# Performance work log

Hardware: AMD Instinct MI355X
Metric: run time of the kernel (lower is better)

## Reference

```python
import jax, jax.numpy as jnp
import numpy as np

EMBED = 1024
FF = 4096
HEADS = 16
HEAD_SIZE = EMBED // HEADS


def setup_inputs() -> dict:
    key = jax.random.key(0)
    ks = jax.random.split(key, 12)
    s = 0.02
    inp = {
        "x": jax.random.normal(ks[0], (2, 2048, EMBED), dtype=jnp.float32),
        "Wq": jax.random.normal(ks[1], (EMBED, EMBED), dtype=jnp.float32) * s,
        "bq": jnp.zeros((EMBED,), jnp.float32),
        "Wk": jax.random.normal(ks[2], (EMBED, EMBED), dtype=jnp.float32) * s,
        "bk": jnp.zeros((EMBED,), jnp.float32),
        "Wv": jax.random.normal(ks[3], (EMBED, EMBED), dtype=jnp.float32) * s,
        "bv": jnp.zeros((EMBED,), jnp.float32),
        "Wo": jax.random.normal(ks[4], (EMBED, EMBED), dtype=jnp.float32) * s,
        "bo": jnp.zeros((EMBED,), jnp.float32),
        "W1": jax.random.normal(ks[5], (EMBED, FF), dtype=jnp.float32) * s,
        "b1": jnp.zeros((FF,), jnp.float32),
        "W2": jax.random.normal(ks[6], (FF, EMBED), dtype=jnp.float32) * s,
        "b2": jnp.zeros((EMBED,), jnp.float32),
        "ln1_g": jnp.ones((EMBED,), jnp.float32),
        "ln1_b": jnp.zeros((EMBED,), jnp.float32),
        "ln2_g": jnp.ones((EMBED,), jnp.float32),
        "ln2_b": jnp.zeros((EMBED,), jnp.float32),
    }
    return inp


def _layernorm(x, g, b, eps=1e-5):
    mu = jnp.mean(x, axis=-1, keepdims=True)
    var = jnp.var(x, axis=-1, keepdims=True)
    return (x - mu) * jax.lax.rsqrt(var + eps) * g + b


def _attn(x, Wq, bq, Wk, bk, Wv, bv, Wo, bo):
    B, S, E = x.shape
    q = (x @ Wq + bq).reshape(B, S, HEADS, HEAD_SIZE)
    k = (x @ Wk + bk).reshape(B, S, HEADS, HEAD_SIZE)
    v = (x @ Wv + bv).reshape(B, S, HEADS, HEAD_SIZE)
    # full (non-causal) attention, scores materialized as in the original
    att = jnp.einsum('bqhd,bkhd->bhqk', q, k) / jnp.sqrt(jnp.float32(HEAD_SIZE))
    att = jax.nn.softmax(att, axis=-1)
    out = jnp.einsum('bhqk,bkhd->bqhd', att, v).reshape(B, S, E)
    return out @ Wo + bo


def reference(x, Wq, bq, Wk, bk, Wv, bv, Wo, bo, W1, b1, W2, b2,
              ln1_g, ln1_b, ln2_g, ln2_b):
    x = x + _attn(_layernorm(x, ln1_g, ln1_b), Wq, bq, Wk, bk, Wv, bv, Wo, bo)
    h = _layernorm(x, ln2_g, ln2_b)
    x = x + (jax.nn.gelu(h @ W1 + b1) @ W2 + b2)
    return x
```

## Files before the change

### kernel.cpp

```cpp
#include <hip/hip_runtime.h>

typedef __bf16 bf16;
typedef __bf16 bf16x8 __attribute__((ext_vector_type(8)));
typedef __bf16 bf16x4 __attribute__((ext_vector_type(4)));
typedef float f32x4 __attribute__((ext_vector_type(4)));

#define EMBED 1024
#define FFDIM 4096
#define HEADS 16
#define HD 64
#define SEQ 2048
#define BATCH 2
#define TOKENS (BATCH * SEQ)
#define MB (1u << 20)


__device__ __forceinline__ void gld16(const void* g, void* l) {
  __builtin_amdgcn_global_load_lds(
      (const __attribute__((address_space(1))) void*)g,
      (__attribute__((address_space(3))) void*)l, 16, 0, 0);
}

__device__ __forceinline__ float gelu_f(float x) {
  float u = 0.7978845608028654f * (x + 0.044715f * x * x * x);
  float t = tanhf(u);
  return 0.5f * x * (1.0f + t);
}

__device__ __forceinline__ void xcd_tiles(int nx, int& tx, int& ty) {
  int lid = blockIdx.x + nx * blockIdx.y;
  tx = (lid >> 3) % nx;
  ty = ((lid / (8 * nx)) << 3) | (lid & 7);
}

__global__ __launch_bounds__(256) void transpose_cast(const float* __restrict__ in,
                                                      bf16* __restrict__ out,
                                                      int R, int C) {
  __shared__ float t[32][33];
  int bx = blockIdx.x * 32;
  int by = blockIdx.y * 32;
  int tx = threadIdx.x & 31;
  int ty = threadIdx.x >> 5;
#pragma unroll
  for (int i = 0; i < 32; i += 8)
    t[ty + i][tx] = in[(size_t)(by + ty + i) * C + bx + tx];
  __syncthreads();
#pragma unroll
  for (int i = 0; i < 32; i += 8)
    out[(size_t)(bx + ty + i) * R + by + tx] = (bf16)t[tx][ty + i];
}

__global__ __launch_bounds__(256) void transpose_cast4(
    const float* __restrict__ W0, const float* __restrict__ W1,
    const float* __restrict__ W2, const float* __restrict__ W3,
    bf16* __restrict__ O0, bf16* __restrict__ O1,
    bf16* __restrict__ O2, bf16* __restrict__ O3) {
  const float* in;
  bf16* out;
  int z = blockIdx.z;
  if (z == 0) { in = W0; out = O0; }
  else if (z == 1) { in = W1; out = O1; }
  else if (z == 2) { in = W2; out = O2; }
  else { in = W3; out = O3; }
  __shared__ float t[32][33];
  int bx = blockIdx.x * 32;
  int by = blockIdx.y * 32;
  int tx = threadIdx.x & 31;
  int ty = threadIdx.x >> 5;
#pragma unroll
  for (int i = 0; i < 32; i += 8)
    t[ty + i][tx] = in[(size_t)(by + ty + i) * EMBED + bx + tx];
  __syncthreads();
#pragma unroll
  for (int i = 0; i < 32; i += 8)
    out[(size_t)(bx + ty + i) * EMBED + by + tx] = (bf16)t[tx][ty + i];
}

__global__ __launch_bounds__(256) void ln_kernel(const float* __restrict__ x,
                                                 const float* __restrict__ g,
                                                 const float* __restrict__ b,
                                                 bf16* __restrict__ out) {
  int tok = blockIdx.x;
  int tid = threadIdx.x;
  const float4* xv = (const float4*)(x + (size_t)tok * EMBED);
  float4 v = xv[tid];
  float s = v.x + v.y + v.z + v.w;
  float s2 = v.x * v.x + v.y * v.y + v.z * v.z + v.w * v.w;
#pragma unroll
  for (int off = 32; off >= 1; off >>= 1) {
    s += __shfl_xor(s, off, 64);
    s2 += __shfl_xor(s2, off, 64);
  }
  __shared__ float ps[4], ps2[4];
  int w = tid >> 6;
  if ((tid & 63) == 0) { ps[w] = s; ps2[w] = s2; }
  __syncthreads();
  s = ps[0] + ps[1] + ps[2] + ps[3];
  s2 = ps2[0] + ps2[1] + ps2[2] + ps2[3];
  float mu = s * (1.0f / EMBED);
  float var = s2 * (1.0f / EMBED) - mu * mu;
  float r = rsqrtf(var + 1e-5f);
  float4 gg = ((const float4*)g)[tid];
  float4 bb = ((const float4*)b)[tid];
  bf16x4 o;
  o[0] = (bf16)((v.x - mu) * r * gg.x + bb.x);
  o[1] = (bf16)((v.y - mu) * r * gg.y + bb.y);
  o[2] = (bf16)((v.z - mu) * r * gg.z + bb.z);
  o[3] = (bf16)((v.w - mu) * r * gg.w + bb.w);
  ((bf16x4*)(out + (size_t)tok * EMBED))[tid] = o;
}

template <int MODE>
__global__ __launch_bounds__(256) void gemm_bt(const bf16* __restrict__ A,
                                               const bf16* __restrict__ BT,
                                               const float* __restrict__ bias,
                                               void* __restrict__ out,
                                               int M, int N, int K,
                                               const float* __restrict__ bias2,
                                               const float* __restrict__ bias3,
                                               void* __restrict__ out2,
                                               void* __restrict__ out3) {
  __shared__ bf16 ldsA[128 * 64];
  __shared__ bf16 ldsB[128 * 64];
  int tid = threadIdx.x;
  int wave = tid >> 6, lane = tid & 63;
  int lquad = lane >> 4, l15 = lane & 15;
  int wm = wave >> 1, wn = wave & 1;
  int tileM = blockIdx.y * 128, tileN = blockIdx.x * 128;

  f32x4 acc[4][4];
#pragma unroll
  for (int i = 0; i < 4; i++)
#pragma unroll
    for (int j = 0; j < 4; j++) acc[i][j] = (f32x4){0.f, 0.f, 0.f, 0.f};

  int srow = lane >> 3;
  int sch = lane & 7;

  for (int k0 = 0; k0 < K; k0 += 64) {
    __syncthreads();
#pragma unroll
    for (int c = 0; c < 4; c++) {
      int base = wave * 32 + c * 8;
      int row = base + srow;
      int ch = sch ^ (row & 7);
      gld16(&A[(size_t)(tileM + row) * K + k0 + ch * 8], &ldsA[base * 64]);
      gld16(&BT[(size_t)(tileN + row) * K + k0 + ch * 8], &ldsB[base * 64]);
    }
    __syncthreads();

    bf16x8 aF[2][4], bF[2][4];
#pragma unroll
    for (int ks = 0; ks < 2; ks++) {
#pragma unroll
      for (int i = 0; i < 4; i++) {
        int R = wm * 64 + i * 16 + l15;
        int ch = (ks * 4 + lquad) ^ (R & 7);
        aF[ks][i] = *(const bf16x8*)&ldsA[R * 64 + ch * 8];
      }
#pragma unroll
      for (int j = 0; j < 4; j++) {
        int R = wn * 64 + j * 16 + l15;
        int ch = (ks * 4 + lquad) ^ (R & 7);
        bF[ks][j] = *(const bf16x8*)&ldsB[R * 64 + ch * 8];
      }
    }
#pragma unroll
    for (int i = 0; i < 4; i++)
#pragma unroll
      for (int j = 0; j < 4; j++)
#pragma unroll
        for (int ks = 0; ks < 2; ks++)
          acc[i][j] = __builtin_amdgcn_mfma_f32_16x16x32_bf16(aF[ks][i], bF[ks][j], acc[i][j], 0, 0, 0);
  }

  int r0 = tileM + wm * 64;
  int c0 = tileN + wn * 64;
#pragma unroll
  for (int i = 0; i < 4; i++) {
#pragma unroll
    for (int j = 0; j < 4; j++) {
      int col = c0 + j * 16 + l15;
      float bv;
      if (MODE == 4) {
        int sel = col >> 10, cc = col & 1023;
        bv = (sel == 0 ? bias : sel == 1 ? bias2 : bias3)[cc];
      } else {
        bv = bias[col];
      }
#pragma unroll
      for (int r = 0; r < 4; r++) {
        int row = r0 + i * 16 + lquad * 4 + r;
        float v = acc[i][j][r] + bv;
        if (MODE == 0) {
          ((bf16*)out)[(size_t)row * N + col] = (bf16)v;
        } else if (MODE == 3) {
          ((bf16*)out)[(size_t)row * N + col] = (bf16)gelu_f(v);
        } else {
          int sel = col >> 10, cc = col & 1023;
          if (sel == 0) {
            ((bf16*)out)[(size_t)row * EMBED + cc] = (bf16)v;
          } else if (sel == 1) {
            ((bf16*)out2)[(size_t)row * EMBED + cc] = (bf16)v;
          } else {
            int bb = row >> 11, s = row & (SEQ - 1);
            ((bf16*)out3)[((size_t)(bb * EMBED + cc)) * SEQ + s] = (bf16)v;
          }
        }
      }
    }
  }
}

__global__ __launch_bounds__(256) void gemm_bt64(const bf16* __restrict__ A,
                                                 const bf16* __restrict__ BT,
                                                 const float* __restrict__ bias,
                                                 const float* __restrict__ res,
                                                 float* __restrict__ out,
                                                 int M, int N, int K) {
  __shared__ bf16 ldsA[128 * 64];
  __shared__ bf16 ldsB[64 * 64];
  int tid = threadIdx.x;
  int wave = tid >> 6, lane = tid & 63;
  int lquad = lane >> 4, l15 = lane & 15;
  int wm = wave >> 1, wn = wave & 1;
  int txs, tys;
  xcd_tiles(N >> 6, txs, tys);
  int tileM = tys * 128, tileN = txs * 64;

  f32x4 acc[4][2];
#pragma unroll
  for (int i = 0; i < 4; i++)
#pragma unroll
    for (int j = 0; j < 2; j++) acc[i][j] = (f32x4){0.f, 0.f, 0.f, 0.f};

  int srow = lane >> 3;
  int sch = lane & 7;

  for (int k0 = 0; k0 < K; k0 += 64) {
    __syncthreads();
#pragma unroll
    for (int c = 0; c < 4; c++) {
      int base = wave * 32 + c * 8;
      int row = base + srow;
      int ch = sch ^ (row & 7);
      gld16(&A[(size_t)(tileM + row) * K + k0 + ch * 8], &ldsA[base * 64]);
    }
#pragma unroll
    for (int c = 0; c < 2; c++) {
      int base = wave * 16 + c * 8;
      int row = base + srow;
      int ch = sch ^ (row & 7);
      gld16(&BT[(size_t)(tileN + row) * K + k0 + ch * 8], &ldsB[base * 64]);
    }
    __syncthreads();

    bf16x8 aF[2][4], bF[2][2];
#pragma unroll
    for (int ks = 0; ks < 2; ks++) {
#pragma unroll
      for (int i = 0; i < 4; i++) {
        int R = wm * 64 + i * 16 + l15;
        int ch = (ks * 4 + lquad) ^ (R & 7);
        aF[ks][i] = *(const bf16x8*)&ldsA[R * 64 + ch * 8];
      }
#pragma unroll
      for (int j = 0; j < 2; j++) {
        int R = wn * 32 + j * 16 + l15;
        int ch = (ks * 4 + lquad) ^ (R & 7);
        bF[ks][j] = *(const bf16x8*)&ldsB[R * 64 + ch * 8];
      }
    }
#pragma unroll
    for (int i = 0; i < 4; i++)
#pragma unroll
      for (int j = 0; j < 2; j++)
#pragma unroll
        for (int ks = 0; ks < 2; ks++)
          acc[i][j] = __builtin_amdgcn_mfma_f32_16x16x32_bf16(aF[ks][i], bF[ks][j], acc[i][j], 0, 0, 0);
  }

  int r0 = tileM + wm * 64;
  int c0 = tileN + wn * 32;
#pragma unroll
  for (int i = 0; i < 4; i++) {
#pragma unroll
    for (int j = 0; j < 2; j++) {
      int col = c0 + j * 16 + l15;
      float bv = bias[col];
#pragma unroll
      for (int r = 0; r < 4; r++) {
        int row = r0 + i * 16 + lquad * 4 + r;
        out[(size_t)row * N + col] = acc[i][j][r] + bv + res[(size_t)row * N + col];
      }
    }
  }
}

__global__ __launch_bounds__(256) void attn_kernel(const bf16* __restrict__ q,
                                                   const bf16* __restrict__ k,
                                                   const bf16* __restrict__ vT,
                                                   bf16* __restrict__ o) {
  int lid = blockIdx.x;
  int qb = (lid >> 3) & 15;
  int g = (lid & 7) | ((lid >> 7) << 3);
  int h = g & 15, b = g >> 4;
  int tid = threadIdx.x;
  int w = tid >> 6, lane = tid & 63;
  int lquad = lane >> 4, l15 = lane & 15;

  __shared__ bf16 ldsK[128 * 64];
  __shared__ bf16 ldsV[64 * 128];
  __shared__ bf16 ldsP[4][16 * 136];

  bf16x8 qB[2][2];
#pragma unroll
  for (int f = 0; f < 2; f++) {
    int qrow = b * SEQ + qb * 128 + w * 32 + f * 16 + l15;
    qB[f][0] = *(const bf16x8*)&q[(size_t)qrow * EMBED + h * HD + lquad * 8];
    qB[f][1] = *(const bf16x8*)&q[(size_t)qrow * EMBED + h * HD + 32 + lquad * 8];
  }

  f32x4 O[2][4];
#pragma unroll
  for (int f = 0; f < 2; f++)
#pragma unroll
    for (int j = 0; j < 4; j++) O[f][j] = (f32x4){0.f, 0.f, 0.f, 0.f};
  float lsum[2] = {0.f, 0.f};
  const float C2 = 0.18033688011112042f;

  for (int kb = 0; kb < SEQ; kb += 128) {
    __syncthreads();
#pragma unroll
    for (int c = 0; c < 4; c++) {
      int base = w * 32 + c * 8;
      int row = base + (lane >> 3);
      int ch = (lane & 7) ^ (row & 7);
      gld16(&k[(size_t)(b * SEQ + kb + row) * EMBED + h * HD + ch * 8],
            &ldsK[base * 64]);
    }
#pragma unroll
    for (int c = 0; c < 4; c++) {
      int base = w * 16 + c * 4;
      int row = base + (lane >> 4);
      int ch = (lane & 15) ^ (row & 7);
      gld16(&vT[(size_t)(b * EMBED + h * HD + row) * SEQ + kb + ch * 8],
            &ldsV[base * 128]);
    }
    __syncthreads();

    f32x4 st[2][8];
#pragma unroll
    for (int t = 0; t < 8; t++) {
      st[0][t] = (f32x4){0.f, 0.f, 0.f, 0.f};
      st[1][t] = (f32x4){0.f, 0.f, 0.f, 0.f};
#pragma unroll
      for (int ks = 0; ks < 2; ks++) {
        int R = t * 16 + l15;
        int ch = (ks * 4 + lquad) ^ (R & 7);
        bf16x8 kA = *(const bf16x8*)&ldsK[R * 64 + ch * 8];
        st[0][t] = __builtin_amdgcn_mfma_f32_16x16x32_bf16(kA, qB[0][ks], st[0][t], 0, 0, 0);
        st[1][t] = __builtin_amdgcn_mfma_f32_16x16x32_bf16(kA, qB[1][ks], st[1][t], 0, 0, 0);
      }
    }

    bf16x8 pB[2][4];
#pragma unroll
    for (int f = 0; f < 2; f++) {
      float rs = 0.f;
#pragma unroll
      for (int t = 0; t < 8; t++) {
        bf16x4 pk;
#pragma unroll
        for (int r = 0; r < 4; r++) {
          float e = __builtin_amdgcn_exp2f(st[f][t][r] * C2);
          rs += e;
          pk[r] = (bf16)e;
        }
        *(bf16x4*)&ldsP[w][l15 * 136 + t * 16 + lquad * 4] = pk;
      }
      lsum[f] += rs;
#pragma unroll
      for (int ks2 = 0; ks2 < 4; ks2++)
        pB[f][ks2] = *(const bf16x8*)&ldsP[w][l15 * 136 + ks2 * 32 + lquad * 8];
    }

#pragma unroll
    for (int j = 0; j < 4; j++) {
#pragma unroll
      for (int ks2 = 0; ks2 < 4; ks2++) {
        int R = j * 16 + l15;
        int ch = (ks2 * 4 + lquad) ^ (R & 7);
        bf16x8 vA = *(const bf16x8*)&ldsV[R * 128 + ch * 8];
        O[0][j] = __builtin_amdgcn_mfma_f32_16x16x32_bf16(vA, pB[0][ks2], O[0][j], 0, 0, 0);
        O[1][j] = __builtin_amdgcn_mfma_f32_16x16x32_bf16(vA, pB[1][ks2], O[1][j], 0, 0, 0);
      }
    }
  }

#pragma unroll
  for (int f = 0; f < 2; f++) {
    float ls = lsum[f];
    ls += __shfl_xor(ls, 16, 64);
    ls += __shfl_xor(ls, 32, 64);
    float inv = 1.0f / ls;
    int tok = b * SEQ + qb * 128 + w * 32 + f * 16 + l15;
#pragma unroll
    for (int j = 0; j < 4; j++) {
      bf16x4 ov;
#pragma unroll
      for (int r = 0; r < 4; r++) ov[r] = (bf16)(O[f][j][r] * inv);
      *(bf16x4*)&o[(size_t)tok * EMBED + h * HD + j * 16 + lquad * 4] = ov;
    }
  }
}


extern "C" void kernel_launch(void* const* d_in, const int* in_sizes, int n_in,
                              void* d_out, int out_size, void* d_ws, size_t ws_size,
                              hipStream_t stream) {
  const float* x = (const float*)d_in[0];
  const float* Wq = (const float*)d_in[1];
  const float* bq = (const float*)d_in[2];
  const float* Wk = (const float*)d_in[3];
  const float* bk = (const float*)d_in[4];
  const float* Wv = (const float*)d_in[5];
  const float* bv = (const float*)d_in[6];
  const float* Wo = (const float*)d_in[7];
  const float* bo = (const float*)d_in[8];
  const float* W1 = (const float*)d_in[9];
  const float* b1 = (const float*)d_in[10];
  const float* W2 = (const float*)d_in[11];
  const float* b2 = (const float*)d_in[12];
  const float* ln1_g = (const float*)d_in[13];
  const float* ln1_b = (const float*)d_in[14];
  const float* ln2_g = (const float*)d_in[15];
  const float* ln2_b = (const float*)d_in[16];

  char* ws = (char*)d_ws;
  bf16* WqT = (bf16*)(ws + 0 * MB);
  bf16* WkT = (bf16*)(ws + 2 * MB);
  bf16* WvT = (bf16*)(ws + 4 * MB);
  bf16* WoT = (bf16*)(ws + 6 * MB);
  bf16* W1T = (bf16*)(ws + 8 * MB);
  bf16* W2T = (bf16*)(ws + 16 * MB);
  bf16* xn1 = (bf16*)(ws + 24 * MB);
  bf16* qbuf = (bf16*)(ws + 32 * MB);
  bf16* kbuf = (bf16*)(ws + 40 * MB);
  bf16* vT = (bf16*)(ws + 48 * MB);
  bf16* attnb = (bf16*)(ws + 56 * MB);
  float* x2f = (float*)(ws + 64 * MB);
  bf16* xn2 = (bf16*)(ws + 80 * MB);
  bf16* hb = (bf16*)(ws + 88 * MB);
  float* outf = (float*)d_out;

  transpose_cast4<<<dim3(32, 32, 4), 256, 0, stream>>>(Wq, Wk, Wv, Wo,
                                                       WqT, WkT, WvT, WoT);
  transpose_cast<<<dim3(128, 32), 256, 0, stream>>>(W1, W1T, EMBED, FFDIM);
  transpose_cast<<<dim3(32, 128), 256, 0, stream>>>(W2, W2T, FFDIM, EMBED);

  ln_kernel<<<TOKENS, 256, 0, stream>>>(x, ln1_g, ln1_b, xn1);

  gemm_bt<4><<<dim3(3072 / 128, TOKENS / 128), 256, 0, stream>>>(
      xn1, WqT, bq, qbuf, TOKENS, 3072, EMBED, bk, bv, kbuf, vT);

  attn_kernel<<<dim3(SEQ / 128 * HEADS * BATCH), 256, 0, stream>>>(qbuf, kbuf, vT, attnb);

  gemm_bt64<<<dim3(EMBED / 64, TOKENS / 128), 256, 0, stream>>>(
      attnb, WoT, bo, x, x2f, TOKENS, EMBED, EMBED);

  ln_kernel<<<TOKENS, 256, 0, stream>>>(x2f, ln2_g, ln2_b, xn2);

  gemm_bt<3><<<dim3(FFDIM / 128, TOKENS / 128), 256, 0, stream>>>(
      xn2, W1T, b1, hb, TOKENS, FFDIM, EMBED,
      nullptr, nullptr, nullptr, nullptr);
  gemm_bt64<<<dim3(EMBED / 64, TOKENS / 128), 256, 0, stream>>>(
      hb, W2T, b2, x2f, outf, TOKENS, EMBED, FFDIM);
}
```

Baseline: 372.7 us.

## Split-K the output GEMMs with atomic accumulation into LN-preinitialized residual buffers

Replaces the 128x64-tile output projection and FFN-down GEMMs with a 128x128-tile split-K (two halves) kernel that atomically adds partial sums into fp32 output. The LayerNorm kernels now also write residual+bias into the destination buffer, so the GEMM epilogue no longer reads the residual or bias. The intent is to raise per-tile reuse while keeping the block count up and to drop the residual reads. In exchange it adds fp32 atomic traffic, makes results depend on summation order, and removes the XCD-aware tile mapping.

```diff
diff --git a/kernel.cpp b/kernel.cpp
--- a/kernel.cpp
+++ b/kernel.cpp
@@ -25,12 +25,6 @@
   float u = 0.7978845608028654f * (x + 0.044715f * x * x * x);
   float t = tanhf(u);
   return 0.5f * x * (1.0f + t);
-}
-
-__device__ __forceinline__ void xcd_tiles(int nx, int& tx, int& ty) {
-  int lid = blockIdx.x + nx * blockIdx.y;
-  tx = (lid >> 3) % nx;
-  ty = ((lid / (8 * nx)) << 3) | (lid & 7);
 }
 
 __global__ __launch_bounds__(256) void transpose_cast(const float* __restrict__ in,
@@ -76,10 +70,12 @@
     out[(size_t)(bx + ty + i) * EMBED + by + tx] = (bf16)t[tx][ty + i];
 }
 
-__global__ __launch_bounds__(256) void ln_kernel(const float* __restrict__ x,
-                                                 const float* __restrict__ g,
-                                                 const float* __restrict__ b,
-                                                 bf16* __restrict__ out) {
+__global__ __launch_bounds__(256) void ln_fused(const float* __restrict__ x,
+                                                const float* __restrict__ g,
+                                                const float* __restrict__ b,
+                                                const float* __restrict__ bias2,
+                                                bf16* __restrict__ out,
+                                                float* __restrict__ init_out) {
   int tok = blockIdx.x;
   int tid = threadIdx.x;
   const float4* xv = (const float4*)(x + (size_t)tok * EMBED);
@@ -108,6 +104,10 @@
   o[2] = (bf16)((v.z - mu) * r * gg.z + bb.z);
   o[3] = (bf16)((v.w - mu) * r * gg.w + bb.w);
   ((bf16x4*)(out + (size_t)tok * EMBED))[tid] = o;
+  float4 i2 = ((const float4*)bias2)[tid];
+  float4 iv;
+  iv.x = v.x + i2.x; iv.y = v.y + i2.y; iv.z = v.z + i2.z; iv.w = v.w + i2.w;
+  ((float4*)(init_out + (size_t)tok * EMBED))[tid] = iv;
 }
 
 template <int MODE>
@@ -192,11 +192,9 @@
       for (int r = 0; r < 4; r++) {
         int row = r0 + i * 16 + lquad * 4 + r;
         float v = acc[i][j][r] + bv;
-        if (MODE == 0) {
-          ((bf16*)out)[(size_t)row * N + col] = (bf16)v;
-        } else if (MODE == 3) {
+        if (MODE == 3) {
           ((bf16*)out)[(size_t)row * N + col] = (bf16)gelu_f(v);
-        } else {
+        } else if (MODE == 4) {
           int sel = col >> 10, cc = col & 1023;
           if (sel == 0) {
             ((bf16*)out)[(size_t)row * EMBED + cc] = (bf16)v;
@@ -206,38 +204,38 @@
             int bb = row >> 11, s = row & (SEQ - 1);
             ((bf16*)out3)[((size_t)(bb * EMBED + cc)) * SEQ + s] = (bf16)v;
           }
+        } else {
+          ((bf16*)out)[(size_t)row * N + col] = (bf16)v;
         }
       }
     }
   }
 }
 
-__global__ __launch_bounds__(256) void gemm_bt64(const bf16* __restrict__ A,
-                                                 const bf16* __restrict__ BT,
-                                                 const float* __restrict__ bias,
-                                                 const float* __restrict__ res,
-                                                 float* __restrict__ out,
-                                                 int M, int N, int K) {
+__global__ __launch_bounds__(256) void gemm_sk(const bf16* __restrict__ A,
+                                               const bf16* __restrict__ BT,
+                                               float* __restrict__ out,
+                                               int M, int N, int K) {
   __shared__ bf16 ldsA[128 * 64];
-  __shared__ bf16 ldsB[64 * 64];
+  __shared__ bf16 ldsB[128 * 64];
   int tid = threadIdx.x;
   int wave = tid >> 6, lane = tid & 63;
   int lquad = lane >> 4, l15 = lane & 15;
   int wm = wave >> 1, wn = wave & 1;
-  int txs, tys;
-  xcd_tiles(N >> 6, txs, tys);
-  int tileM = tys * 128, tileN = txs * 64;
-
-  f32x4 acc[4][2];
+  int tileM = blockIdx.y * 128, tileN = blockIdx.x * 128;
+  int Kh = K >> 1;
+  int kbeg = blockIdx.z * Kh;
+
+  f32x4 acc[4][4];
 #pragma unroll
   for (int i = 0; i < 4; i++)
 #pragma unroll
-    for (int j = 0; j < 2; j++) acc[i][j] = (f32x4){0.f, 0.f, 0.f, 0.f};
+    for (int j = 0; j < 4; j++) acc[i][j] = (f32x4){0.f, 0.f, 0.f, 0.f};
 
   int srow = lane >> 3;
   int sch = lane & 7;
 
-  for (int k0 = 0; k0 < K; k0 += 64) {
+  for (int k0 = kbeg; k0 < kbeg + Kh; k0 += 64) {
     __syncthreads();
 #pragma unroll
     for (int c = 0; c < 4; c++) {
@@ -245,17 +243,11 @@
       int row = base + srow;
       int ch = sch ^ (row & 7);
       gld16(&A[(size_t)(tileM + row) * K + k0 + ch * 8], &ldsA[base * 64]);
-    }
-#pragma unroll
-    for (int c = 0; c < 2; c++) {
-      int base = wave * 16 + c * 8;
-      int row = base + srow;
-      int ch = sch ^ (row & 7);
       gld16(&BT[(size_t)(tileN + row) * K + k0 + ch * 8], &ldsB[base * 64]);
     }
     __syncthreads();
 
-    bf16x8 aF[2][4], bF[2][2];
+    bf16x8 aF[2][4], bF[2][4];
 #pragma unroll
     for (int ks = 0; ks < 2; ks++) {
 #pragma unroll
@@ -265,8 +257,8 @@
         aF[ks][i] = *(const bf16x8*)&ldsA[R * 64 + ch * 8];
       }
 #pragma unroll
-      for (int j = 0; j < 2; j++) {
-        int R = wn * 32 + j * 16 + l15;
+      for (int j = 0; j < 4; j++) {
+        int R = wn * 64 + j * 16 + l15;
         int ch = (ks * 4 + lquad) ^ (R & 7);
         bF[ks][j] = *(const bf16x8*)&ldsB[R * 64 + ch * 8];
       }
@@ -274,24 +266,23 @@
 #pragma unroll
     for (int i = 0; i < 4; i++)
 #pragma unroll
-      for (int j = 0; j < 2; j++)
+      for (int j = 0; j < 4; j++)
 #pragma unroll
         for (int ks = 0; ks < 2; ks++)
           acc[i][j] = __builtin_amdgcn_mfma_f32_16x16x32_bf16(aF[ks][i], bF[ks][j], acc[i][j], 0, 0, 0);
   }
 
   int r0 = tileM + wm * 64;
-  int c0 = tileN + wn * 32;
+  int c0 = tileN + wn * 64;
 #pragma unroll
   for (int i = 0; i < 4; i++) {
 #pragma unroll
-    for (int j = 0; j < 2; j++) {
+    for (int j = 0; j < 4; j++) {
       int col = c0 + j * 16 + l15;
-      float bv = bias[col];
 #pragma unroll
       for (int r = 0; r < 4; r++) {
         int row = r0 + i * 16 + lquad * 4 + r;
-        out[(size_t)row * N + col] = acc[i][j][r] + bv + res[(size_t)row * N + col];
+        atomicAdd(&out[(size_t)row * N + col], acc[i][j][r]);
       }
     }
   }
@@ -459,21 +450,22 @@
   transpose_cast<<<dim3(128, 32), 256, 0, stream>>>(W1, W1T, EMBED, FFDIM);
   transpose_cast<<<dim3(32, 128), 256, 0, stream>>>(W2, W2T, FFDIM, EMBED);
 
-  ln_kernel<<<TOKENS, 256, 0, stream>>>(x, ln1_g, ln1_b, xn1);
+  ln_fused<<<TOKENS, 256, 0, stream>>>(x, ln1_g, ln1_b, bo, xn1, x2f);
 
   gemm_bt<4><<<dim3(3072 / 128, TOKENS / 128), 256, 0, stream>>>(
       xn1, WqT, bq, qbuf, TOKENS, 3072, EMBED, bk, bv, kbuf, vT);
 
   attn_kernel<<<dim3(SEQ / 128 * HEADS * BATCH), 256, 0, stream>>>(qbuf, kbuf, vT, attnb);
 
-  gemm_bt64<<<dim3(EMBED / 64, TOKENS / 128), 256, 0, stream>>>(
-      attnb, WoT, bo, x, x2f, TOKENS, EMBED, EMBED);
-
-  ln_kernel<<<TOKENS, 256, 0, stream>>>(x2f, ln2_g, ln2_b, xn2);
+  gemm_sk<<<dim3(EMBED / 128, TOKENS / 128, 2), 256, 0, stream>>>(
+      attnb, WoT, x2f, TOKENS, EMBED, EMBED);
+
+  ln_fused<<<TOKENS, 256, 0, stream>>>(x2f, ln2_g, ln2_b, b2, xn2, outf);
 
   gemm_bt<3><<<dim3(FFDIM / 128, TOKENS / 128), 256, 0, stream>>>(
       xn2, W1T, b1, hb, TOKENS, FFDIM, EMBED,
       nullptr, nullptr, nullptr, nullptr);
-  gemm_bt64<<<dim3(EMBED / 64, TOKENS / 128), 256, 0, stream>>>(
-      hb, W2T, b2, x2f, outf, TOKENS, EMBED, FFDIM);
-}
+
+  gemm_sk<<<dim3(EMBED / 128, TOKENS / 128, 2), 256, 0, stream>>>(
+      hb, W2T, outf, TOKENS, EMBED, FFDIM);
+}
```

After: 400.8 us. +7.6%, slower.
